# Optimization experiments

Hardware: AMD Instinct MI355X
Metric: run time of the kernel (lower is better)

## Reference

```python
import jax, jax.numpy as jnp
import numpy as np

EMBED = 768
HIDDEN = 3072
HEADS = 12
EPS = 1e-6


def _ln(x, g, b):
    mu = jnp.mean(x, axis=-1, keepdims=True)
    var = jnp.mean(jnp.square(x - mu), axis=-1, keepdims=True)
    return (x - mu) / jnp.sqrt(var + EPS) * g + b


def setup_inputs() -> dict:
    key = jax.random.key(0)
    ks = jax.random.split(key, 12)
    s = lambda fan_in: 1.0 / np.sqrt(fan_in)
    x = jax.random.normal(ks[0], (16, 1024, EMBED), dtype=jnp.float32)
    return {
        "x": x,
        "ln1_g": jnp.ones((EMBED,), jnp.float32),
        "ln1_b": jnp.zeros((EMBED,), jnp.float32),
        "qkv_w": jax.random.uniform(ks[1], (3 * EMBED, EMBED), jnp.float32, -s(EMBED), s(EMBED)),
        "qkv_b": jax.random.uniform(ks[2], (3 * EMBED,), jnp.float32, -s(EMBED), s(EMBED)),
        "proj_w": jax.random.uniform(ks[3], (EMBED, EMBED), jnp.float32, -s(EMBED), s(EMBED)),
        "proj_b": jax.random.uniform(ks[4], (EMBED,), jnp.float32, -s(EMBED), s(EMBED)),
        "ln2_g": jnp.ones((EMBED,), jnp.float32),
        "ln2_b": jnp.zeros((EMBED,), jnp.float32),
        "fc1_w": jax.random.uniform(ks[5], (HIDDEN, EMBED), jnp.float32, -s(EMBED), s(EMBED)),
        "fc1_b": jax.random.uniform(ks[6], (HIDDEN,), jnp.float32, -s(EMBED), s(EMBED)),
        "fc2_w": jax.random.uniform(ks[7], (EMBED, HIDDEN), jnp.float32, -s(HIDDEN), s(HIDDEN)),
        "fc2_b": jax.random.uniform(ks[8], (EMBED,), jnp.float32, -s(HIDDEN), s(HIDDEN)),
    }


def reference(x, ln1_g, ln1_b, qkv_w, qkv_b, proj_w, proj_b, ln2_g, ln2_b, fc1_w, fc1_b, fc2_w, fc2_b):
    B, N, D = x.shape
    Hd = D // HEADS
    scale = Hd ** -0.5
    # attention branch
    xn = _ln(x, ln1_g, ln1_b)
    qkv = xn @ qkv_w.T + qkv_b  # [B,N,3D]
    qkv = qkv.reshape(B, N, 3, HEADS, Hd).transpose(2, 0, 3, 1, 4)
    q, k, v = qkv[0], qkv[1], qkv[2]  # [B,H,N,Hd]
    attn = jax.nn.softmax(jnp.einsum("bhqd,bhkd->bhqk", q, k) * scale, axis=-1)
    ctx = jnp.einsum("bhqk,bhkd->bhqd", attn, v)
    ctx = ctx.transpose(0, 2, 1, 3).reshape(B, N, D)
    x = x + ctx @ proj_w.T + proj_b
    # MLP branch
    h = _ln(x, ln2_g, ln2_b)
    h = jax.nn.gelu(h @ fc1_w.T + fc1_b, approximate=False)
    x = x + h @ fc2_w.T + fc2_b
    return x
```

## Files before the change

### kernel.cpp

```cpp
#include <hip/hip_runtime.h>
#include <math.h>


typedef unsigned short u16;
typedef __attribute__((ext_vector_type(8))) short bf16x8;
typedef __attribute__((ext_vector_type(4))) float f32x4;

#define MFMA_BF16(a, b, c) __builtin_amdgcn_mfma_f32_16x16x32_bf16((a), (b), (c), 0, 0, 0)

__device__ __forceinline__ float bf2f(u16 v) {
    return __uint_as_float(((unsigned)v) << 16);
}
__device__ __forceinline__ u16 f2bf(float f) {
    unsigned u = __float_as_uint(f);
    u += 0x7fffu + ((u >> 16) & 1u);
    return (u16)(u >> 16);
}

__device__ __forceinline__ float gelu_fast(float v) {
    const float t = v * v;
    const float z = v * (1.5957691216f + 0.0713548162f * t);
    const float e = __expf(-z);
    return v * __builtin_amdgcn_rcpf(1.0f + e);
}

typedef __attribute__((address_space(1))) const void gvoid;
typedef __attribute__((address_space(3))) void lvoid;
__device__ __forceinline__ void gll16(const void* g, void* l) {
    __builtin_amdgcn_global_load_lds((gvoid*)g, (lvoid*)l, 16, 0, 0);
}

__global__ __launch_bounds__(256) void cast32(const float* __restrict__ src,
                                              u16* __restrict__ dst, int n8) {
    const int i = blockIdx.x * 256 + threadIdx.x;
    if (i >= n8) return;
    const float4 a = ((const float4*)src)[2 * i];
    const float4 b = ((const float4*)src)[2 * i + 1];
    bf16x8 r;
    r[0] = (short)f2bf(a.x); r[1] = (short)f2bf(a.y);
    r[2] = (short)f2bf(a.z); r[3] = (short)f2bf(a.w);
    r[4] = (short)f2bf(b.x); r[5] = (short)f2bf(b.y);
    r[6] = (short)f2bf(b.z); r[7] = (short)f2bf(b.w);
    ((bf16x8*)dst)[i] = r;
}

__global__ __launch_bounds__(256) void ln_kernel(const float* __restrict__ x,
                                                 const float* __restrict__ g,
                                                 const float* __restrict__ b,
                                                 u16* __restrict__ out) {
    const int row = blockIdx.x;
    const int t = threadIdx.x;
    const float* xr = x + (size_t)row * 768;
    float v0 = xr[t], v1 = xr[t + 256], v2 = xr[t + 512];
    float s = v0 + v1 + v2;
    float sq = v0 * v0 + v1 * v1 + v2 * v2;
#pragma unroll
    for (int off = 32; off > 0; off >>= 1) {
        s += __shfl_down(s, off);
        sq += __shfl_down(sq, off);
    }
    __shared__ float red_s[4], red_sq[4], sh_mu, sh_rs;
    const int wave = t >> 6, lane = t & 63;
    if (lane == 0) { red_s[wave] = s; red_sq[wave] = sq; }
    __syncthreads();
    if (t == 0) {
        float S = red_s[0] + red_s[1] + red_s[2] + red_s[3];
        float SQ = red_sq[0] + red_sq[1] + red_sq[2] + red_sq[3];
        float mu = S * (1.0f / 768.0f);
        float var = SQ * (1.0f / 768.0f) - mu * mu;
        sh_mu = mu;
        sh_rs = 1.0f / sqrtf(fmaxf(var, 0.0f) + 1e-6f);
    }
    __syncthreads();
    const float mu = sh_mu, rs = sh_rs;
    u16* orow = out + (size_t)row * 768;
    orow[t]       = f2bf((v0 - mu) * rs * g[t]       + b[t]);
    orow[t + 256] = f2bf((v1 - mu) * rs * g[t + 256] + b[t + 256]);
    orow[t + 512] = f2bf((v2 - mu) * rs * g[t + 512] + b[t + 512]);
}

template <int EPI, int BF16B>
__global__ __launch_bounds__(256, 2) void gemm2(
        const u16* __restrict__ A, const void* __restrict__ Bv,
        const float* __restrict__ bias, const float* __restrict__ res,
        void* __restrict__ Cv, u16* __restrict__ vtb, int N, int K) {
    __shared__ __align__(16) u16 As[128 * 32];
    __shared__ __align__(16) u16 Bs[128 * 32];
    const int t = threadIdx.x;
    const int wave = t >> 6, lane = t & 63;
    const int quad = lane >> 4, mr = lane & 15;
    const int wm = wave >> 1, wn = wave & 1;
    const int m0 = blockIdx.y * 128;
    const int n0 = blockIdx.x * 128;

    f32x4 acc[4][4];
#pragma unroll
    for (int i = 0; i < 4; i++)
#pragma unroll
        for (int j = 0; j < 4; j++) acc[i][j] = (f32x4){0.f, 0.f, 0.f, 0.f};

    const int seg = wave * 2;
    const int drow = lane >> 2;
    const int dcol = (lane & 3) * 8;
    const int sr = t >> 2, skv = t & 3;

    for (int k0 = 0; k0 < K; k0 += 32) {
#pragma unroll
        for (int c = 0; c < 2; c++) {
            const int rowA = (seg + c) * 16 + drow;
            gll16(A + (size_t)(m0 + rowA) * K + k0 + dcol, &As[(seg + c) * 512]);
        }
        if (BF16B) {
            const u16* Bh = (const u16*)Bv;
#pragma unroll
            for (int c = 0; c < 2; c++) {
                const int rowB = (seg + c) * 16 + drow;
                gll16(Bh + (size_t)(n0 + rowB) * K + k0 + dcol, &Bs[(seg + c) * 512]);
            }
        } else {
            const float* Bf = (const float*)Bv;
#pragma unroll
            for (int half = 0; half < 2; half++) {
                const float* src = Bf + (size_t)(n0 + sr + half * 64) * K + k0 + skv * 8;
                const float4 a = *(const float4*)src;
                const float4 b2 = *(const float4*)(src + 4);
                bf16x8 r;
                r[0] = (short)f2bf(a.x);  r[1] = (short)f2bf(a.y);
                r[2] = (short)f2bf(a.z);  r[3] = (short)f2bf(a.w);
                r[4] = (short)f2bf(b2.x); r[5] = (short)f2bf(b2.y);
                r[6] = (short)f2bf(b2.z); r[7] = (short)f2bf(b2.w);
                *(bf16x8*)&Bs[(sr + half * 64) * 32 + skv * 8] = r;
            }
        }
        __syncthreads();
        bf16x8 af[4], bfr[4];
#pragma unroll
        for (int i = 0; i < 4; i++)
            af[i] = *(const bf16x8*)&As[(wm * 64 + i * 16 + mr) * 32 + quad * 8];
#pragma unroll
        for (int j = 0; j < 4; j++)
            bfr[j] = *(const bf16x8*)&Bs[(wn * 64 + j * 16 + mr) * 32 + quad * 8];
#pragma unroll
        for (int i = 0; i < 4; i++)
#pragma unroll
            for (int j = 0; j < 4; j++)
                acc[i][j] = MFMA_BF16(af[i], bfr[j], acc[i][j]);
        __syncthreads();
    }

#pragma unroll
    for (int i = 0; i < 4; i++) {
#pragma unroll
        for (int r = 0; r < 4; r++) {
            const int m = m0 + wm * 64 + i * 16 + quad * 4 + r;
#pragma unroll
            for (int j = 0; j < 4; j++) {
                const int n = n0 + wn * 64 + j * 16 + mr;
                float v = acc[i][j][r] + bias[n];
                if (EPI == 1) {
                    v = gelu_fast(v);
                    ((u16*)Cv)[(size_t)m * N + n] = f2bf(v);
                } else if (EPI == 2) {
                    v += res[(size_t)m * N + n];
                    ((float*)Cv)[(size_t)m * N + n] = v;
                } else {
                    if (n < 1536) {
                        const float vq = (n < 768) ? v * 0.125f : v;
                        ((u16*)Cv)[(size_t)m * 1536 + n] = f2bf(vq);
                    } else {
                        const int h = (n - 1536) >> 6, hd = (n - 1536) & 63;
                        const int bb = m >> 10, pos = m & 1023;
                        vtb[((size_t)(bb * 12 + h) * 64 + hd) * 1024 + pos] = f2bf(v);
                    }
                }
            }
        }
    }
}

#define AFRAG(T, ROW, KS) \
    (*(const bf16x8*)&(T)[(ROW)][(((((KS) << 2) | quad)) ^ ((ROW) & 7)) << 3])

template <int EPI>
__global__ __launch_bounds__(512, 2) void gemm8(
        const u16* __restrict__ A, const u16* __restrict__ Bw,
        const float* __restrict__ bias, const float* __restrict__ res,
        void* __restrict__ Cv, u16* __restrict__ vtb, int N, int K) {
    __shared__ __align__(16) u16 As[2][256][64];
    __shared__ __align__(16) u16 Bs[2][256][64];
    const int t = threadIdx.x;
    const int wave = t >> 6, lane = t & 63;
    const int quad = lane >> 4, mr = lane & 15;
    const int wm = wave >> 2, wn = wave & 3;
    const int m0 = blockIdx.y * 256, n0 = blockIdx.x * 256;
    const int NT = K >> 6;

    const int srow = wave * 8 + (lane >> 3);
    const int sgrp = ((lane & 7) ^ (lane >> 3)) * 8;

#define STAGE_A(BI, SLOT, KT)                                                   \
    gll16(A + (size_t)(m0 + (SLOT) * 64 + srow) * K + (KT) * 64 + sgrp,         \
          &As[BI][(SLOT) * 64 + wave * 8][0])
#define STAGE_B(BI, SLOT, KT)                                                   \
    gll16(Bw + (size_t)(n0 + (SLOT) * 64 + srow) * K + (KT) * 64 + sgrp,        \
          &Bs[BI][(SLOT) * 64 + wave * 8][0])

#pragma unroll
    for (int s = 0; s < 4; s++) STAGE_A(0, s, 0);
#pragma unroll
    for (int s = 0; s < 4; s++) STAGE_B(0, s, 0);
    STAGE_A(1, 0, 1);
    STAGE_A(1, 2, 1);

    f32x4 acc[8][4];
#pragma unroll
    for (int i = 0; i < 8; i++)
#pragma unroll
        for (int j = 0; j < 4; j++) acc[i][j] = (f32x4){0.f, 0.f, 0.f, 0.f};

    asm volatile("s_waitcnt vmcnt(2)" ::: "memory");
    __builtin_amdgcn_s_barrier();
    asm volatile("" ::: "memory");

    for (int kt = 0; kt < NT; ++kt) {
        const int bi = kt & 1;
        const u16(*Ab)[64] = As[bi];
        const u16(*Bb)[64] = Bs[bi];
        const bool st1 = (kt + 1 < NT);
        const bool st2 = (kt + 2 < NT);
        bf16x8 af[4], bfv[4];

#pragma unroll
        for (int i = 0; i < 4; i++) af[i] = AFRAG(Ab, wm * 128 + i * 16 + mr, 0);
#pragma unroll
        for (int j = 0; j < 4; j++) bfv[j] = AFRAG(Bb, wn * 64 + j * 16 + mr, 0);
        if (st1) { STAGE_B(bi ^ 1, 0, kt + 1); STAGE_B(bi ^ 1, 1, kt + 1); }
        asm volatile("" ::: "memory");
        __builtin_amdgcn_s_barrier();
        asm volatile("" ::: "memory");
        __builtin_amdgcn_s_setprio(1);
#pragma unroll
        for (int i = 0; i < 4; i++)
#pragma unroll
            for (int j = 0; j < 4; j++)
                acc[i][j] = MFMA_BF16(af[i], bfv[j], acc[i][j]);
        __builtin_amdgcn_s_setprio(0);
        asm volatile("" ::: "memory");
        __builtin_amdgcn_s_barrier();
        asm volatile("" ::: "memory");

#pragma unroll
        for (int i = 0; i < 4; i++) af[i] = AFRAG(Ab, wm * 128 + 64 + i * 16 + mr, 0);
        if (st1) { STAGE_B(bi ^ 1, 2, kt + 1); STAGE_B(bi ^ 1, 3, kt + 1); }
        asm volatile("" ::: "memory");
        __builtin_amdgcn_s_barrier();
        asm volatile("" ::: "memory");
        __builtin_amdgcn_s_setprio(1);
#pragma unroll
        for (int i = 0; i < 4; i++)
#pragma unroll
            for (int j = 0; j < 4; j++)
                acc[4 + i][j] = MFMA_BF16(af[i], bfv[j], acc[4 + i][j]);
        __builtin_amdgcn_s_setprio(0);
        asm volatile("" ::: "memory");
        __builtin_amdgcn_s_barrier();
        asm volatile("" ::: "memory");

#pragma unroll
        for (int i = 0; i < 4; i++) af[i] = AFRAG(Ab, wm * 128 + i * 16 + mr, 1);
#pragma unroll
        for (int j = 0; j < 4; j++) bfv[j] = AFRAG(Bb, wn * 64 + j * 16 + mr, 1);
        if (st1) { STAGE_A(bi ^ 1, 1, kt + 1); STAGE_A(bi ^ 1, 3, kt + 1); }
        asm volatile("" ::: "memory");
        __builtin_amdgcn_s_barrier();
        asm volatile("" ::: "memory");
        __builtin_amdgcn_s_setprio(1);
#pragma unroll
        for (int i = 0; i < 4; i++)
#pragma unroll
            for (int j = 0; j < 4; j++)
                acc[i][j] = MFMA_BF16(af[i], bfv[j], acc[i][j]);
        __builtin_amdgcn_s_setprio(0);
        asm volatile("" ::: "memory");
        __builtin_amdgcn_s_barrier();
        asm volatile("" ::: "memory");

#pragma unroll
        for (int i = 0; i < 4; i++) af[i] = AFRAG(Ab, wm * 128 + 64 + i * 16 + mr, 1);
        if (st2) { STAGE_A(bi, 0, kt + 2); STAGE_A(bi, 2, kt + 2); }
        asm volatile("" ::: "memory");
        __builtin_amdgcn_s_barrier();
        asm volatile("" ::: "memory");
        __builtin_amdgcn_s_setprio(1);
#pragma unroll
        for (int i = 0; i < 4; i++)
#pragma unroll
            for (int j = 0; j < 4; j++)
                acc[4 + i][j] = MFMA_BF16(af[i], bfv[j], acc[4 + i][j]);
        __builtin_amdgcn_s_setprio(0);
        if (st2) {
            asm volatile("s_waitcnt vmcnt(2)" ::: "memory");
        } else if (st1) {
            asm volatile("s_waitcnt vmcnt(0)" ::: "memory");
        }
        asm volatile("" ::: "memory");
        __builtin_amdgcn_s_barrier();
        asm volatile("" ::: "memory");
    }

#pragma unroll
    for (int i = 0; i < 8; i++) {
#pragma unroll
        for (int r = 0; r < 4; r++) {
            const int m = m0 + wm * 128 + i * 16 + quad * 4 + r;
#pragma unroll
            for (int j = 0; j < 4; j++) {
                const int n = n0 + wn * 64 + j * 16 + mr;
                float v = acc[i][j][r] + bias[n];
                if (EPI == 1) {
                    v = gelu_fast(v);
                    ((u16*)Cv)[(size_t)m * N + n] = f2bf(v);
                } else if (EPI == 2) {
                    v += res[(size_t)m * N + n];
                    ((float*)Cv)[(size_t)m * N + n] = v;
                } else {
                    if (n < 1536) {
                        const float vq = (n < 768) ? v * 0.125f : v;
                        ((u16*)Cv)[(size_t)m * 1536 + n] = f2bf(vq);
                    } else {
                        const int h = (n - 1536) >> 6, hd = (n - 1536) & 63;
                        const int bb = m >> 10, pos = m & 1023;
                        vtb[((size_t)(bb * 12 + h) * 64 + hd) * 1024 + pos] = f2bf(v);
                    }
                }
            }
        }
    }
#undef STAGE_A
#undef STAGE_B
}

__global__ __launch_bounds__(256) void attn2(const u16* __restrict__ qkkb,
                                             const u16* __restrict__ vtb,
                                             u16* __restrict__ ctx) {
    __shared__ __align__(16) u16 Ks[2][64][72];
    __shared__ __align__(16) u16 Vt[2][64][72];
    __shared__ __align__(16) u16 Ps[64][72];
    const int bh = blockIdx.y;
    const int b = bh / 12, h = bh % 12;
    const int q0 = blockIdx.x * 64;
    const int t = threadIdx.x;
    const int wave = t >> 6, lane = t & 63, quad = lane >> 4, mr = lane & 15;

    const u16* qrow = qkkb + (size_t)(b * 1024 + q0 + wave * 16 + mr) * 1536 + h * 64;
    const bf16x8 qf0 = *(const bf16x8*)(qrow + quad * 8);
    const bf16x8 qf1 = *(const bf16x8*)(qrow + 32 + quad * 8);

    const u16* kbase = qkkb + (size_t)b * 1024 * 1536 + 768 + h * 64;
    const u16* vbase = vtb + (size_t)bh * 64 * 1024;

    const int srow = t >> 3;
    const int sv = t & 7;

    f32x4 oacc[4];
#pragma unroll
    for (int j = 0; j < 4; j++) oacc[j] = (f32x4){0.f, 0.f, 0.f, 0.f};
    float lsum[4] = {0.f, 0.f, 0.f, 0.f};

    bf16x8 pk0, pk1, pv0, pv1;
    pk0 = *(const bf16x8*)(kbase + (size_t)(srow)      * 1536 + sv * 8);
    pk1 = *(const bf16x8*)(kbase + (size_t)(srow + 32) * 1536 + sv * 8);
    pv0 = *(const bf16x8*)(vbase + (size_t)(srow)      * 1024 + sv * 8);
    pv1 = *(const bf16x8*)(vbase + (size_t)(srow + 32) * 1024 + sv * 8);
    *(bf16x8*)&Ks[0][srow][sv * 8] = pk0;
    *(bf16x8*)&Ks[0][srow + 32][sv * 8] = pk1;
    *(bf16x8*)&Vt[0][srow][sv * 8] = pv0;
    *(bf16x8*)&Vt[0][srow + 32][sv * 8] = pv1;

    for (int kt = 0; kt < 16; ++kt) {
        __syncthreads();
        const int cur = kt & 1;
        if (kt < 15) {
            const size_t ko = (size_t)(kt + 1) * 64;
            pk0 = *(const bf16x8*)(kbase + (ko + srow)      * 1536 + sv * 8);
            pk1 = *(const bf16x8*)(kbase + (ko + srow + 32) * 1536 + sv * 8);
            pv0 = *(const bf16x8*)(vbase + (size_t)(srow)      * 1024 + ko + sv * 8);
            pv1 = *(const bf16x8*)(vbase + (size_t)(srow + 32) * 1024 + ko + sv * 8);
        }
        f32x4 sf[4];
#pragma unroll
        for (int j = 0; j < 4; j++) {
            const bf16x8 kf0 = *(const bf16x8*)&Ks[cur][j * 16 + mr][quad * 8];
            const bf16x8 kf1 = *(const bf16x8*)&Ks[cur][j * 16 + mr][32 + quad * 8];
            f32x4 s = (f32x4){0.f, 0.f, 0.f, 0.f};
            s = MFMA_BF16(qf0, kf0, s);
            s = MFMA_BF16(qf1, kf1, s);
            sf[j] = s;
        }
#pragma unroll
        for (int r = 0; r < 4; r++) {
            const float p0 = __expf(sf[0][r] - 8.0f);
            const float p1 = __expf(sf[1][r] - 8.0f);
            const float p2 = __expf(sf[2][r] - 8.0f);
            const float p3 = __expf(sf[3][r] - 8.0f);
            lsum[r] += (p0 + p1) + (p2 + p3);
            const int prow = wave * 16 + quad * 4 + r;
            Ps[prow][0 * 16 + mr] = f2bf(p0);
            Ps[prow][1 * 16 + mr] = f2bf(p1);
            Ps[prow][2 * 16 + mr] = f2bf(p2);
            Ps[prow][3 * 16 + mr] = f2bf(p3);
        }
        __asm__ __volatile__("s_waitcnt lgkmcnt(0)" ::: "memory");
#pragma unroll
        for (int st = 0; st < 2; st++) {
            const bf16x8 pf = *(const bf16x8*)&Ps[wave * 16 + mr][st * 32 + quad * 8];
#pragma unroll
            for (int j = 0; j < 4; j++) {
                const bf16x8 vf = *(const bf16x8*)&Vt[cur][j * 16 + mr][st * 32 + quad * 8];
                oacc[j] = MFMA_BF16(pf, vf, oacc[j]);
            }
        }
        if (kt < 15) {
            const int nxt = cur ^ 1;
            *(bf16x8*)&Ks[nxt][srow][sv * 8] = pk0;
            *(bf16x8*)&Ks[nxt][srow + 32][sv * 8] = pk1;
            *(bf16x8*)&Vt[nxt][srow][sv * 8] = pv0;
            *(bf16x8*)&Vt[nxt][srow + 32][sv * 8] = pv1;
        }
    }

#pragma unroll
    for (int r = 0; r < 4; r++) {
#pragma unroll
        for (int off = 1; off < 16; off <<= 1) lsum[r] += __shfl_xor(lsum[r], off);
        const float inv = 1.0f / lsum[r];
        u16* dst = ctx + (size_t)(b * 1024 + q0 + wave * 16 + quad * 4 + r) * 768 + h * 64;
#pragma unroll
        for (int j = 0; j < 4; j++) dst[j * 16 + mr] = f2bf(oacc[j][r] * inv);
    }
}

extern "C" void kernel_launch(void* const* d_in, const int* in_sizes, int n_in,
                              void* d_out, int out_size, void* d_ws, size_t ws_size,
                              hipStream_t stream) {
    const float* x      = (const float*)d_in[0];
    const float* ln1_g  = (const float*)d_in[1];
    const float* ln1_b  = (const float*)d_in[2];
    const float* qkv_w  = (const float*)d_in[3];
    const float* qkv_b  = (const float*)d_in[4];
    const float* proj_w = (const float*)d_in[5];
    const float* proj_b = (const float*)d_in[6];
    const float* ln2_g  = (const float*)d_in[7];
    const float* ln2_b  = (const float*)d_in[8];
    const float* fc1_w  = (const float*)d_in[9];
    const float* fc1_b  = (const float*)d_in[10];
    const float* fc2_w  = (const float*)d_in[11];
    const float* fc2_b  = (const float*)d_in[12];
    float* out = (float*)d_out;

    char* base = (char*)d_ws + 1024;
    u16* xn   = (u16*)base;
    u16* qkkb = (u16*)(base + 25165824);
    u16* vtb  = (u16*)(base + 75497472);
    u16* h1   = (u16*)(base + 25165824);
    u16* ctxb = xn;
    u16* hn   = xn;

    const size_t WOFF = 125830144ull;
    const bool big = ws_size >= 139985920ull;
    u16* wqkv  = (u16*)((char*)d_ws + WOFF);
    u16* wproj = (u16*)((char*)d_ws + WOFF + 3538944);
    u16* wfc1  = (u16*)((char*)d_ws + WOFF + 4718592);
    u16* wfc2  = (u16*)((char*)d_ws + WOFF + 9437184);

    if (big) {
        cast32<<<dim3(864),  dim3(256), 0, stream>>>(qkv_w,  wqkv,  221184);
        cast32<<<dim3(288),  dim3(256), 0, stream>>>(proj_w, wproj, 73728);
        cast32<<<dim3(1152), dim3(256), 0, stream>>>(fc1_w,  wfc1,  294912);
        cast32<<<dim3(1152), dim3(256), 0, stream>>>(fc2_w,  wfc2,  294912);
    }

    ln_kernel<<<dim3(16384), dim3(256), 0, stream>>>(x, ln1_g, ln1_b, xn);

    if (big)
        gemm8<3><<<dim3(9, 64), dim3(512), 0, stream>>>(
            xn, wqkv, qkv_b, nullptr, qkkb, vtb, 2304, 768);
    else
        gemm2<3, 0><<<dim3(18, 128), dim3(256), 0, stream>>>(
            xn, qkv_w, qkv_b, nullptr, qkkb, vtb, 2304, 768);

    attn2<<<dim3(16, 192), dim3(256), 0, stream>>>(qkkb, vtb, ctxb);

    if (big)
        gemm2<2, 1><<<dim3(6, 128), dim3(256), 0, stream>>>(
            ctxb, wproj, proj_b, x, out, nullptr, 768, 768);
    else
        gemm2<2, 0><<<dim3(6, 128), dim3(256), 0, stream>>>(
            ctxb, proj_w, proj_b, x, out, nullptr, 768, 768);

    ln_kernel<<<dim3(16384), dim3(256), 0, stream>>>(out, ln2_g, ln2_b, hn);

    if (big)
        gemm8<1><<<dim3(12, 64), dim3(512), 0, stream>>>(
            hn, wfc1, fc1_b, nullptr, h1, nullptr, 3072, 768);
    else
        gemm2<1, 0><<<dim3(24, 128), dim3(256), 0, stream>>>(
            hn, fc1_w, fc1_b, nullptr, h1, nullptr, 3072, 768);

    if (big)
        gemm8<2><<<dim3(3, 64), dim3(512), 0, stream>>>(
            h1, wfc2, fc2_b, out, out, nullptr, 768, 3072);
    else
        gemm2<2, 0><<<dim3(6, 128), dim3(256), 0, stream>>>(
            h1, fc2_w, fc2_b, out, out, nullptr, 768, 3072);
}
```

Measured before the change: 618.3 us.

## Deepen gemm8 prefetch pipeline, add XCD block remap, use gemm8 for proj

Reorders the global-to-LDS staging in gemm8 so the next tile's B half and A half are issued earlier, with finer vmcnt waits that let compute start once the first A slots arrive. Adds a block-id swizzle that groups consecutive workgroups across the 8 XCDs for better L2 reuse. Routes the attention output projection through the 256x256 gemm8 kernel instead of gemm2. Risks include wait-count mistakes and fewer blocks (192) for the proj GEMM.

```diff
diff --git a/kernel.cpp b/kernel.cpp
--- a/kernel.cpp
+++ b/kernel.cpp
@@ -7,6 +7,8 @@
 typedef __attribute__((ext_vector_type(4))) float f32x4;
 
 #define MFMA_BF16(a, b, c) __builtin_amdgcn_mfma_f32_16x16x32_bf16((a), (b), (c), 0, 0, 0)
+#define MEMFENCE asm volatile("" ::: "memory")
+#define WAITV(N) asm volatile("s_waitcnt vmcnt(" #N ")" ::: "memory")
 
 __device__ __forceinline__ float bf2f(u16 v) {
     return __uint_as_float(((unsigned)v) << 16);
@@ -192,7 +194,11 @@
     const int wave = t >> 6, lane = t & 63;
     const int quad = lane >> 4, mr = lane & 15;
     const int wm = wave >> 2, wn = wave & 3;
-    const int m0 = blockIdx.y * 256, n0 = blockIdx.x * 256;
+    const int gx = gridDim.x;
+    const int nwg = gx * gridDim.y;
+    int bid = blockIdx.y * gx + blockIdx.x;
+    bid = (bid & 7) * (nwg >> 3) + (bid >> 3);
+    const int m0 = (bid / gx) * 256, n0 = (bid % gx) * 256;
     const int NT = K >> 6;
 
     const int srow = wave * 8 + (lane >> 3);
@@ -205,12 +211,11 @@
     gll16(Bw + (size_t)(n0 + (SLOT) * 64 + srow) * K + (KT) * 64 + sgrp,        \
           &Bs[BI][(SLOT) * 64 + wave * 8][0])
 
-#pragma unroll
-    for (int s = 0; s < 4; s++) STAGE_A(0, s, 0);
-#pragma unroll
-    for (int s = 0; s < 4; s++) STAGE_B(0, s, 0);
-    STAGE_A(1, 0, 1);
-    STAGE_A(1, 2, 1);
+    STAGE_A(0, 0, 0); STAGE_A(0, 2, 0);
+    STAGE_B(0, 0, 0); STAGE_B(0, 1, 0);
+    STAGE_B(0, 2, 0); STAGE_B(0, 3, 0);
+    STAGE_A(0, 1, 0); STAGE_A(0, 3, 0);
+    if (NT > 1) { STAGE_A(1, 0, 1); STAGE_A(1, 2, 1); STAGE_B(1, 0, 1); STAGE_B(1, 1, 1); }
 
     f32x4 acc[8][4];
 #pragma unroll
@@ -218,9 +223,9 @@
 #pragma unroll
         for (int j = 0; j < 4; j++) acc[i][j] = (f32x4){0.f, 0.f, 0.f, 0.f};
 
-    asm volatile("s_waitcnt vmcnt(2)" ::: "memory");
+    if (NT > 1) { WAITV(6); } else { WAITV(2); }
     __builtin_amdgcn_s_barrier();
-    asm volatile("" ::: "memory");
+    MEMFENCE;
 
     for (int kt = 0; kt < NT; ++kt) {
         const int bi = kt & 1;
@@ -234,10 +239,10 @@
         for (int i = 0; i < 4; i++) af[i] = AFRAG(Ab, wm * 128 + i * 16 + mr, 0);
 #pragma unroll
         for (int j = 0; j < 4; j++) bfv[j] = AFRAG(Bb, wn * 64 + j * 16 + mr, 0);
-        if (st1) { STAGE_B(bi ^ 1, 0, kt + 1); STAGE_B(bi ^ 1, 1, kt + 1); }
-        asm volatile("" ::: "memory");
-        __builtin_amdgcn_s_barrier();
-        asm volatile("" ::: "memory");
+        if (st1) { STAGE_B(bi ^ 1, 2, kt + 1); STAGE_B(bi ^ 1, 3, kt + 1); }
+        MEMFENCE;
+        __builtin_amdgcn_s_barrier();
+        MEMFENCE;
         __builtin_amdgcn_s_setprio(1);
 #pragma unroll
         for (int i = 0; i < 4; i++)
@@ -245,16 +250,17 @@
             for (int j = 0; j < 4; j++)
                 acc[i][j] = MFMA_BF16(af[i], bfv[j], acc[i][j]);
         __builtin_amdgcn_s_setprio(0);
-        asm volatile("" ::: "memory");
-        __builtin_amdgcn_s_barrier();
-        asm volatile("" ::: "memory");
+        if (st1) { WAITV(6); } else { WAITV(0); }
+        MEMFENCE;
+        __builtin_amdgcn_s_barrier();
+        MEMFENCE;
 
 #pragma unroll
         for (int i = 0; i < 4; i++) af[i] = AFRAG(Ab, wm * 128 + 64 + i * 16 + mr, 0);
-        if (st1) { STAGE_B(bi ^ 1, 2, kt + 1); STAGE_B(bi ^ 1, 3, kt + 1); }
-        asm volatile("" ::: "memory");
-        __builtin_amdgcn_s_barrier();
-        asm volatile("" ::: "memory");
+        if (st1) { STAGE_A(bi ^ 1, 1, kt + 1); STAGE_A(bi ^ 1, 3, kt + 1); }
+        MEMFENCE;
+        __builtin_amdgcn_s_barrier();
+        MEMFENCE;
         __builtin_amdgcn_s_setprio(1);
 #pragma unroll
         for (int i = 0; i < 4; i++)
@@ -262,18 +268,17 @@
             for (int j = 0; j < 4; j++)
                 acc[4 + i][j] = MFMA_BF16(af[i], bfv[j], acc[4 + i][j]);
         __builtin_amdgcn_s_setprio(0);
-        asm volatile("" ::: "memory");
-        __builtin_amdgcn_s_barrier();
-        asm volatile("" ::: "memory");
+        MEMFENCE;
+        __builtin_amdgcn_s_barrier();
+        MEMFENCE;
 
 #pragma unroll
         for (int i = 0; i < 4; i++) af[i] = AFRAG(Ab, wm * 128 + i * 16 + mr, 1);
 #pragma unroll
         for (int j = 0; j < 4; j++) bfv[j] = AFRAG(Bb, wn * 64 + j * 16 + mr, 1);
-        if (st1) { STAGE_A(bi ^ 1, 1, kt + 1); STAGE_A(bi ^ 1, 3, kt + 1); }
-        asm volatile("" ::: "memory");
-        __builtin_amdgcn_s_barrier();
-        asm volatile("" ::: "memory");
+        MEMFENCE;
+        __builtin_amdgcn_s_barrier();
+        MEMFENCE;
         __builtin_amdgcn_s_setprio(1);
 #pragma unroll
         for (int i = 0; i < 4; i++)
@@ -281,16 +286,17 @@
             for (int j = 0; j < 4; j++)
                 acc[i][j] = MFMA_BF16(af[i], bfv[j], acc[i][j]);
         __builtin_amdgcn_s_setprio(0);
-        asm volatile("" ::: "memory");
-        __builtin_amdgcn_s_barrier();
-        asm volatile("" ::: "memory");
+        MEMFENCE;
+        __builtin_amdgcn_s_barrier();
+        MEMFENCE;
 
 #pragma unroll
         for (int i = 0; i < 4; i++) af[i] = AFRAG(Ab, wm * 128 + 64 + i * 16 + mr, 1);
-        if (st2) { STAGE_A(bi, 0, kt + 2); STAGE_A(bi, 2, kt + 2); }
-        asm volatile("" ::: "memory");
-        __builtin_amdgcn_s_barrier();
-        asm volatile("" ::: "memory");
+        if (st2) { STAGE_A(bi, 0, kt + 2); STAGE_A(bi, 2, kt + 2);
+                   STAGE_B(bi, 0, kt + 2); STAGE_B(bi, 1, kt + 2); }
+        MEMFENCE;
+        __builtin_amdgcn_s_barrier();
+        MEMFENCE;
         __builtin_amdgcn_s_setprio(1);
 #pragma unroll
         for (int i = 0; i < 4; i++)
@@ -298,14 +304,10 @@
             for (int j = 0; j < 4; j++)
                 acc[4 + i][j] = MFMA_BF16(af[i], bfv[j], acc[4 + i][j]);
         __builtin_amdgcn_s_setprio(0);
-        if (st2) {
-            asm volatile("s_waitcnt vmcnt(2)" ::: "memory");
-        } else if (st1) {
-            asm volatile("s_waitcnt vmcnt(0)" ::: "memory");
-        }
-        asm volatile("" ::: "memory");
-        __builtin_amdgcn_s_barrier();
-        asm volatile("" ::: "memory");
+        if (st2) { WAITV(6); } else if (st1) { WAITV(2); }
+        MEMFENCE;
+        __builtin_amdgcn_s_barrier();
+        MEMFENCE;
     }
 
 #pragma unroll
@@ -492,7 +494,7 @@
     attn2<<<dim3(16, 192), dim3(256), 0, stream>>>(qkkb, vtb, ctxb);
 
     if (big)
-        gemm2<2, 1><<<dim3(6, 128), dim3(256), 0, stream>>>(
+        gemm8<2><<<dim3(3, 64), dim3(512), 0, stream>>>(
             ctxb, wproj, proj_b, x, out, nullptr, 768, 768);
     else
         gemm2<2, 0><<<dim3(6, 128), dim3(256), 0, stream>>>(
```

Measured after the change: 613.9 us. About the same (-0.7%).
